# Kernel optimization log

Hardware: AMD Instinct MI355X
Metric: run time of the kernel (lower is better)

Reference implementation:

```python
import jax, jax.numpy as jnp
import numpy as np

MIN_, MAX_, KSZ, IGNORE_IDX = 10, 10, 3, -255
B, H, W = 256, 256, 256
LI_MAX_ITERS = 64


def setup_inputs() -> dict:
    key = jax.random.key(0)
    x = jax.random.uniform(key, (B, 1, H, W), dtype=jnp.float32)
    return {"x": x}


def _otsu(hist):
    # hist: [256] counts. Returns Otsu threshold (bin value); fg = img > t.
    bins = jnp.arange(256, dtype=jnp.float32)
    w0 = jnp.cumsum(hist)[:-1]
    w1 = hist.sum() - w0
    s0 = jnp.cumsum(hist * bins)[:-1]
    s_tot = (hist * bins).sum()
    m0 = s0 / jnp.maximum(w0, 1e-12)
    m1 = (s_tot - s0) / jnp.maximum(w1, 1e-12)
    var_b = w0 * w1 * (m0 - m1) ** 2
    return jnp.argmax(var_b).astype(jnp.float32)


def _li(hist, init_t):
    # Histogram-based Li iterative minimum cross-entropy threshold
    # (skimage.filters.threshold_li with initial_guess=init_t).
    bins = jnp.arange(256, dtype=jnp.float32)
    img_min = jnp.min(jnp.where(hist > 0, bins, 255.0))
    vals = bins - img_min  # shift so values >= 0 (as skimage does)
    csum = jnp.cumsum(hist)
    cvsum = jnp.cumsum(hist * vals)
    n_tot, s_tot = csum[-1], cvsum[-1]
    tol = 0.5  # integer image -> half the minimal value spacing

    def body(state):
        t_curr, _, i = state
        # background: img <= t_curr + img_min
        idx = jnp.clip(jnp.floor(t_curr + img_min).astype(jnp.int32), 0, 255)
        n_back, s_back = csum[idx], cvsum[idx]
        n_fore, s_fore = n_tot - n_back, s_tot - s_back
        mean_back = jnp.where(n_back > 0, s_back / jnp.maximum(n_back, 1.0), 0.0)
        mean_fore = s_fore / jnp.maximum(n_fore, 1.0)
        eps = 1e-12
        t_next = (mean_back - mean_fore) / (
            jnp.log(jnp.maximum(mean_back, eps)) - jnp.log(jnp.maximum(mean_fore, eps)))
        t_next = jnp.where(mean_back < eps, mean_fore / 2.0, t_next)
        return (t_next, t_curr, i + 1)

    def cond(state):
        t_curr, t_prev, i = state
        return (jnp.abs(t_curr - t_prev) > tol) & (i < LI_MAX_ITERS)

    t0 = init_t - img_min
    t_fin, _, _ = jax.lax.while_loop(cond, body, (t0, t0 + 10.0, 0))
    return t_fin + img_min


def _sample_mask(key, region, k):
    # Uniform sampling without replacement of up to k pixels from region
    # (bool [H,W]) via random-score top-k (equiv. to torch.multinomial
    # with uniform probs, w/o replacement).
    flat = region.reshape(-1)
    scores = jnp.where(flat, jax.random.uniform(key, (flat.shape[0],)), -1.0)
    top, idx = jax.lax.top_k(scores, k)
    valid = (top >= 0.0).astype(jnp.int32)
    mask = jnp.zeros(flat.shape[0], jnp.int32).at[idx].max(valid)
    return mask.reshape(region.shape)


def _dilate(m):
    # kornia dilation with ones (KSZ,KSZ) kernel on a 0/1 mask == max filter.
    return jax.lax.reduce_window(m, 0, jax.lax.max, (KSZ, KSZ), (1, 1), "SAME")


def _per_image(img_u8, key_fg, key_bg):
    # img_u8: [H,W] int32 in [0,255]
    hist = jnp.zeros(256, jnp.float32).at[img_u8.ravel()].add(1.0)
    otsu = jnp.clip(_otsu(hist), 1.0, 254.0)  # clamp 0->1, 255->254
    li_t = _li(hist, otsu)
    roi = img_u8.astype(jnp.float32) > li_t

    fg = _sample_mask(key_fg, roi, MAX_)
    bg = _sample_mask(key_bg, jnp.logical_not(roi), MIN_)
    if KSZ > 1:
        fg = _dilate(fg)
        bg = _dilate(bg)

    overlap = (fg + bg) == 2
    fg = jnp.where(overlap, 0, fg)
    bg = jnp.where(overlap, 0, bg)

    seeds = jnp.full((H, W), IGNORE_IDX, jnp.int32)
    seeds = jnp.where(bg == 1, 0, seeds)
    seeds = jnp.where(fg == 1, 1, seeds)
    return seeds


def reference(x):
    b = x.shape[0]
    # (cam*255).astype(uint8): truncation, cam in [0,1]
    img = jnp.clip(jnp.floor(x[:, 0] * 255.0), 0, 255).astype(jnp.int32)
    keys = jax.random.split(jax.random.key(1), (b, 2))
    return jax.vmap(_per_image)(img, keys[:, 0], keys[:, 1])
```

## Files before the change

### kernel.cpp

```cpp
#include <hip/hip_runtime.h>
#include <stdint.h>

#define NPIX 65536
#define IGN (-255)
#define CAPB 96

typedef unsigned long long u64;
typedef int v4i __attribute__((ext_vector_type(4)));

__device__ __forceinline__ uint32_t rotl32(uint32_t v, uint32_t r){ return (v<<r)|(v>>(32u-r)); }

__device__ __forceinline__ void tf2x32(uint32_t k0, uint32_t k1, uint32_t x0, uint32_t x1,
                                       uint32_t &o0, uint32_t &o1){
  uint32_t k2 = k0 ^ k1 ^ 0x1BD11BDAu;
  x0 += k0; x1 += k1;
#define TFR(r) { x0 += x1; x1 = rotl32(x1,(r)); x1 ^= x0; }
  TFR(13u) TFR(15u) TFR(26u) TFR(6u)   x0 += k1; x1 += k2 + 1u;
  TFR(17u) TFR(29u) TFR(16u) TFR(24u)  x0 += k2; x1 += k0 + 2u;
  TFR(13u) TFR(15u) TFR(26u) TFR(6u)   x0 += k0; x1 += k1 + 3u;
  TFR(17u) TFR(29u) TFR(16u) TFR(24u)  x0 += k1; x1 += k2 + 4u;
  TFR(13u) TFR(15u) TFR(26u) TFR(6u)   x0 += k2; x1 += k0 + 5u;
#undef TFR
  o0 = x0; o1 = x1;
}

__device__ __forceinline__ uint32_t tf_bits(uint32_t k0, uint32_t k1, uint32_t k2, uint32_t pix){
  uint32_t x0 = k0, x1 = pix + k1;
#define TFR(r) { x0 += x1; x1 = rotl32(x1,(r)); x1 ^= x0; }
  TFR(13u) TFR(15u) TFR(26u) TFR(6u)   x0 += k1; x1 += k2 + 1u;
  TFR(17u) TFR(29u) TFR(16u) TFR(24u)  x0 += k2; x1 += k0 + 2u;
  TFR(13u) TFR(15u) TFR(26u) TFR(6u)   x0 += k0; x1 += k1 + 3u;
  TFR(17u) TFR(29u) TFR(16u) TFR(24u)  x0 += k1; x1 += k2 + 4u;
  TFR(13u) TFR(15u) TFR(26u) TFR(6u)   x0 += k2; x1 += k0 + 5u;
#undef TFR
  return x0 ^ x1;
}

__device__ __forceinline__ u64 packCand(uint32_t bits, uint32_t pix){
  float f = __uint_as_float((bits >> 9) | 0x3f800000u) - 1.0f;
  uint32_t u = __float_as_uint(f) ^ 0x80000000u;
  return ((u64)u << 32) | (u64)(0xFFFFFFFFu - pix);
}

__device__ __forceinline__ void t10_insert(u64* l, u64 c){
  if (c > l[9]) {
    l[9] = c;
#pragma unroll
    for (int i = 9; i > 0; --i){
      u64 a = l[i-1], b2 = l[i];
      if (b2 > a){ l[i-1] = b2; l[i] = a; }
    }
  }
}

__global__ __launch_bounds__(256)
void k1_hist(const float* __restrict__ x, uint32_t* __restrict__ phist,
             uint32_t* __restrict__ u8c){
  const int img = blockIdx.x >> 3;
  const int chk = blockIdx.x & 7;
  const int tid = threadIdx.x;
  const float4* x4 = (const float4*)(x + (size_t)img * NPIX);

  __shared__ uint32_t h4[1024];
  h4[tid] = 0u; h4[tid+256] = 0u; h4[tid+512] = 0u; h4[tid+768] = 0u;
  __syncthreads();

  const int sub = tid & 3;
#pragma unroll
  for (int j = 0; j < 8; ++j){
    int p4 = chk*2048 + j*256 + tid;
    float4 v = x4[p4];
    uint32_t q0 = (uint32_t)min(max((int)floorf(v.x*255.0f),0),255);
    uint32_t q1 = (uint32_t)min(max((int)floorf(v.y*255.0f),0),255);
    uint32_t q2 = (uint32_t)min(max((int)floorf(v.z*255.0f),0),255);
    uint32_t q3 = (uint32_t)min(max((int)floorf(v.w*255.0f),0),255);
    u8c[(size_t)img*16384 + p4] = q0 | (q1<<8) | (q2<<16) | (q3<<24);
    atomicAdd(&h4[q0*4+sub],1u); atomicAdd(&h4[q1*4+sub],1u);
    atomicAdd(&h4[q2*4+sub],1u); atomicAdd(&h4[q3*4+sub],1u);
  }
  __syncthreads();
  phist[(size_t)(img*8+chk)*256 + tid] = h4[tid*4] + h4[tid*4+1] + h4[tid*4+2] + h4[tid*4+3];
}

__global__ __launch_bounds__(256)
void k1b_thresh(const uint32_t* __restrict__ phist, uint32_t* __restrict__ qcutp,
                uint32_t* __restrict__ nroip){
  const int img = blockIdx.x;
  const int tid = threadIdx.x;

  __shared__ float csum[256], cvsum[256];
  __shared__ u64 s_best;
  __shared__ int s_imin;

  if (tid == 0){ s_imin = 255; s_best = 0ull; }
  uint32_t h = 0;
#pragma unroll
  for (int k = 0; k < 8; ++k) h += phist[(size_t)(img*8+k)*256 + tid];
  __syncthreads();
  if (h) atomicMin(&s_imin, tid);
  __syncthreads();
  const float img_min = (float)s_imin;
  csum[tid]  = (float)h;
  cvsum[tid] = (float)h * ((float)tid - img_min);
  __syncthreads();
  for (int off = 1; off < 256; off <<= 1){
    float a = 0.f, c2 = 0.f;
    if (tid >= off){ a = csum[tid-off]; c2 = cvsum[tid-off]; }
    __syncthreads();
    if (tid >= off){ csum[tid] += a; cvsum[tid] += c2; }
    __syncthreads();
  }
  {
    float s_tot_o = cvsum[255] + img_min * csum[255];
    if (tid < 255){
      float w0 = csum[tid], w1 = 65536.0f - w0;
      float cs = cvsum[tid] + img_min * csum[tid];
      float m0 = cs / fmaxf(w0, 1e-12f);
      float m1 = (s_tot_o - cs) / fmaxf(w1, 1e-12f);
      float d = m0 - m1;
      float vb = (w0*w1) * (d*d);
      u64 pk = ((u64)__float_as_uint(vb) << 32) | (u64)(255 - tid);
      atomicMax(&s_best, pk);
    }
  }
  __syncthreads();
  if (tid == 0){
    int bestIdx = 255 - (int)(s_best & 0xFFFFFFFFull);
    float otsu = fminf(fmaxf((float)bestIdx, 1.0f), 254.0f);
    float n_tot = csum[255], s_tot = cvsum[255];
    float t_curr = otsu - img_min, t_prev = t_curr + 10.0f;
    int it = 0;
    while (fabsf(t_curr - t_prev) > 0.5f && it < 64){
      int idx = min(max((int)floorf(t_curr + img_min), 0), 255);
      float n_back = csum[idx], s_back = cvsum[idx];
      float n_fore = n_tot - n_back, s_fore = s_tot - s_back;
      float mean_back = (n_back > 0.0f) ? (s_back / fmaxf(n_back, 1.0f)) : 0.0f;
      float mean_fore = s_fore / fmaxf(n_fore, 1.0f);
      float t_next = (mean_back - mean_fore) /
                     (logf(fmaxf(mean_back, 1e-12f)) - logf(fmaxf(mean_fore, 1e-12f)));
      if (mean_back < 1e-12f) t_next = mean_fore * 0.5f;
      t_prev = t_curr; t_curr = t_next; ++it;
    }
    float lit = t_curr + img_min;
    int qcut = (int)floorf(lit) + 1;
    uint32_t nroi;
    if (qcut <= 0)        nroi = NPIX;
    else if (qcut > 255)  nroi = 0u;
    else                  nroi = NPIX - (uint32_t)csum[qcut-1];
    qcutp[img] = (uint32_t)qcut;
    nroip[img] = nroi;
  }
}

__global__ __launch_bounds__(256)
void k2_score(const uint32_t* __restrict__ u8c, int* __restrict__ out,
              const uint32_t* __restrict__ qcutp, uint32_t* __restrict__ bcnt,
              u64* __restrict__ cand){
  const int img = blockIdx.x >> 3;
  const int chk = blockIdx.x & 7;
  const int tid = threadIdx.x;

  __shared__ uint32_t s_kw[4], s_cnt[2];
  __shared__ u64 s_cand[2][CAPB];

  if (tid < 2){
    uint32_t o0, o1;
    tf2x32(0u, 1u, 0u, (uint32_t)(2*img + tid), o0, o1);
    s_kw[2*tid] = o0; s_kw[2*tid+1] = o1;
  }
  if (tid == 0){ s_cnt[0] = 0u; s_cnt[1] = 0u; }
  const int qcut = (int)qcutp[img];
  __syncthreads();

  {
    v4i* o4 = (v4i*)(out + (size_t)img * NPIX);
    const v4i f4 = {IGN, IGN, IGN, IGN};
#pragma unroll
    for (int j = 0; j < 8; ++j)
      __builtin_nontemporal_store(f4, &o4[chk*2048 + j*256 + tid]);
  }

  const uint32_t fk0 = s_kw[0], fk1 = s_kw[1], bk0 = s_kw[2], bk1 = s_kw[3];
  const uint32_t fk2 = fk0 ^ fk1 ^ 0x1BD11BDAu;
  const uint32_t bk2 = bk0 ^ bk1 ^ 0x1BD11BDAu;
  const uint4* u4 = (const uint4*)(u8c + (size_t)img*16384);
#pragma unroll
  for (int j = 0; j < 2; ++j){
    int wi = chk*512 + j*256 + tid;
    uint4 w4 = u4[wi];
    uint32_t pix0 = (uint32_t)(wi*16);
    uint32_t ws4[4] = {w4.x, w4.y, w4.z, w4.w};
#pragma unroll
    for (int wsub = 0; wsub < 4; ++wsub){
      uint32_t w = ws4[wsub];
#pragma unroll
      for (int s = 0; s < 4; ++s){
        int q = (int)((w >> (8*s)) & 255u);
        bool r = (q >= qcut);
        uint32_t pix = pix0 + (uint32_t)(wsub*4 + s);
        uint32_t bits = tf_bits(r?fk0:bk0, r?fk1:bk1, r?fk2:bk2, pix);
        if (bits >= 0xFF000000u){
          int r2 = r ? 0 : 1;
          uint32_t idx = atomicAdd(&s_cnt[r2], 1u);
          if (idx < CAPB) s_cand[r2][idx] = packCand(bits, pix);
        }
      }
    }
  }
  __syncthreads();
  if (tid < 2) bcnt[(size_t)(img*8+chk)*2 + tid] = s_cnt[tid];
  {
    int s = tid >> 7, idx = tid & 127;
    int n = min((int)s_cnt[s], CAPB);
    if (idx < n) cand[((size_t)(img*8+chk)*2 + s)*CAPB + idx] = s_cand[s][idx];
  }
}

__global__ __launch_bounds__(256)
void k3_final(const float* __restrict__ x, int* __restrict__ out,
              const uint32_t* __restrict__ qcutp, const uint32_t* __restrict__ nroip,
              const uint32_t* __restrict__ bcnt, const u64* __restrict__ cand){
  const int img = blockIdx.x;
  const int tid = threadIdx.x;

  __shared__ u64 sbuf[2560];
  __shared__ u64 s_top[2][10];
  __shared__ int s_off[2][9], s_fail[2];
  __shared__ uint32_t s_kw[4];
  __shared__ int s_pr[2][10], s_pc[2][10], s_np[2];

  if (tid < 2){
    uint32_t o0, o1;
    tf2x32(0u, 1u, 0u, (uint32_t)(2*img + tid), o0, o1);
    s_kw[2*tid] = o0; s_kw[2*tid+1] = o1;
  }
  if (tid == 0){
    uint32_t nroi = nroip[img];
    for (int s = 0; s < 2; ++s){
      int off = 0, fail = 0;
      for (int k = 0; k < 8; ++k){
        uint32_t raw = bcnt[(size_t)(img*8+k)*2 + s];
        if (raw > (uint32_t)CAPB) fail = 1;
        int ck = (int)min(raw, (uint32_t)CAPB);
        s_off[s][k] = off; off += ck;
      }
      s_off[s][8] = off;
      int region = s ? (int)(NPIX - nroi) : (int)nroi;
      if (off < 10 && off != region) fail = 1;
      s_fail[s] = fail;
    }
  }
  __syncthreads();

  {
    int s = tid >> 7, idx = tid & 127;
#pragma unroll
    for (int k = 0; k < 8; ++k){
      int ck = s_off[s][k+1] - s_off[s][k];
      if (idx < ck) sbuf[s*1280 + s_off[s][k] + idx] = cand[((size_t)(img*8+k)*2 + s)*CAPB + idx];
    }
  }
  __syncthreads();
  if (tid == 0 || tid == 128){
    int s = tid >> 7;
    if (!s_fail[s]){
      u64 t[10];
#pragma unroll
      for (int i = 0; i < 10; ++i) t[i] = 0ull;
      int n = s_off[s][8];
      for (int i = 0; i < n; ++i) t10_insert(t, sbuf[s*1280 + i]);
#pragma unroll
      for (int i = 0; i < 10; ++i) s_top[s][i] = t[i];
    }
  }
  __syncthreads();

  const int qcut = (int)qcutp[img];
  for (int s = 0; s < 2; ++s){
    if (!s_fail[s]) continue;
    uint32_t kk0 = s_kw[2*s], kk1 = s_kw[2*s+1], kk2 = kk0 ^ kk1 ^ 0x1BD11BDAu;
    u64 t[10];
#pragma unroll
    for (int i = 0; i < 10; ++i) t[i] = 0ull;
    for (int k = 0; k < 256; ++k){
      uint32_t pix = (uint32_t)(tid + 256*k);
      float v = x[(size_t)img*NPIX + pix];
      int q = min(max((int)floorf(v*255.0f),0),255);
      bool r = (q >= qcut);
      if (r == (s == 0)) t10_insert(t, packCand(tf_bits(kk0, kk1, kk2, pix), pix));
    }
#pragma unroll
    for (int i = 0; i < 10; ++i) sbuf[tid*10 + i] = t[i];
    __syncthreads();
    if (tid == 0){
      u64 m[10];
#pragma unroll
      for (int i = 0; i < 10; ++i) m[i] = 0ull;
      for (int i = 0; i < 2560; ++i) t10_insert(m, sbuf[i]);
#pragma unroll
      for (int i = 0; i < 10; ++i) s_top[s][i] = m[i];
    }
    __syncthreads();
  }

  if (tid < 2){
    int np = 0;
    for (int i = 0; i < 10; ++i){
      u64 e = s_top[tid][i];
      if (e){
        uint32_t pix = 0xFFFFFFFFu - (uint32_t)(e & 0xFFFFFFFFull);
        s_pr[tid][np] = (int)(pix >> 8);
        s_pc[tid][np] = (int)(pix & 255u);
        ++np;
      }
    }
    s_np[tid] = np;
  }
  __syncthreads();

  int* outb = out + (size_t)img * NPIX;
  const int nfg = s_np[0], nbg = s_np[1];
  const int npts = nfg + nbg;
  if (tid < npts*9){
    int k = tid / 9, d = tid - k*9;
    int pr = (k < nfg) ? s_pr[0][k] : s_pr[1][k - nfg];
    int pc = (k < nfg) ? s_pc[0][k] : s_pc[1][k - nfg];
    pr += d/3 - 1; pc += d%3 - 1;
    if (pr >= 0 && pr < 256 && pc >= 0 && pc < 256){
      bool fgd = false, bgd = false;
      for (int i = 0; i < nfg; ++i) fgd |= (abs(pr - s_pr[0][i]) <= 1) && (abs(pc - s_pc[0][i]) <= 1);
      for (int i = 0; i < nbg; ++i) bgd |= (abs(pr - s_pr[1][i]) <= 1) && (abs(pc - s_pc[1][i]) <= 1);
      int val = (fgd && bgd) ? IGN : (fgd ? 1 : 0);
      outb[pr*256 + pc] = val;
    }
  }
}

__global__ __launch_bounds__(1024, 4)
void apm_fused(const float* __restrict__ x, int* __restrict__ out){
  const int b = blockIdx.x;
  const int tid = threadIdx.x;
  const float* img = x + (size_t)b * NPIX;
  int* outb = out + (size_t)b * NPIX;

  __shared__ uint32_t hist[256];
  __shared__ float csum[256], cvsum[256];
  __shared__ u64 buf[2][256];
  __shared__ uint32_t s_kw[4];
  __shared__ int s_cnt[2];
  __shared__ int s_nroi, s_imin;
  __shared__ u64 s_best;
  __shared__ float s_lit;
  __shared__ int s_fail[2];
  __shared__ int s_pr[2][10], s_pc[2][10], s_np[2];

  if (tid < 256) hist[tid] = 0u;
  if (tid == 0){ s_cnt[0] = 0; s_cnt[1] = 0; s_nroi = 0; s_imin = 255; s_best = 0ull; }
  if (tid < 2){
    uint32_t o0, o1;
    tf2x32(0u, 1u, 0u, (uint32_t)(2*b + tid), o0, o1);
    s_kw[2*tid] = o0; s_kw[2*tid+1] = o1;
  }
  __syncthreads();

  uint32_t packed[16];
  {
    v4i f4 = {IGN, IGN, IGN, IGN};
    const float4* x4 = (const float4*)img;
    v4i* o4 = (v4i*)outb;
#pragma unroll
    for (int j = 0; j < 16; ++j){
      int p4 = tid + 1024*j;
      float4 v = x4[p4];
      o4[p4] = f4;
      uint32_t u0 = (uint32_t)min(max((int)floorf(v.x*255.0f),0),255);
      uint32_t u1 = (uint32_t)min(max((int)floorf(v.y*255.0f),0),255);
      uint32_t u2 = (uint32_t)min(max((int)floorf(v.z*255.0f),0),255);
      uint32_t u3 = (uint32_t)min(max((int)floorf(v.w*255.0f),0),255);
      packed[j] = u0 | (u1<<8) | (u2<<16) | (u3<<24);
      atomicAdd(&hist[u0],1u); atomicAdd(&hist[u1],1u);
      atomicAdd(&hist[u2],1u); atomicAdd(&hist[u3],1u);
    }
  }
  __syncthreads();
  if (tid < 256 && hist[tid]) atomicMin(&s_imin, tid);
  __syncthreads();
  const float img_min = (float)s_imin;
  if (tid < 256){
    float h = (float)hist[tid];
    csum[tid]  = h;
    cvsum[tid] = h * ((float)tid - img_min);
  }
  __syncthreads();
  for (int off = 1; off < 256; off <<= 1){
    float a = 0.f, c2 = 0.f;
    if (tid < 256 && tid >= off){ a = csum[tid-off]; c2 = cvsum[tid-off]; }
    __syncthreads();
    if (tid < 256 && tid >= off){ csum[tid] += a; cvsum[tid] += c2; }
    __syncthreads();
  }
  {
    float s_tot_o = cvsum[255] + img_min * csum[255];
    if (tid < 255){
      float w0 = csum[tid], w1 = 65536.0f - w0;
      float cs = cvsum[tid] + img_min * csum[tid];
      float m0 = cs / fmaxf(w0, 1e-12f);
      float m1 = (s_tot_o - cs) / fmaxf(w1, 1e-12f);
      float d = m0 - m1;
      float vb = (w0*w1) * (d*d);
      u64 pk = ((u64)__float_as_uint(vb) << 32) | (u64)(255 - tid);
      atomicMax(&s_best, pk);
    }
  }
  __syncthreads();
  if (tid == 0){
    int bestIdx = 255 - (int)(s_best & 0xFFFFFFFFull);
    float otsu = fminf(fmaxf((float)bestIdx, 1.0f), 254.0f);
    float n_tot = csum[255], s_tot = cvsum[255];
    float t_curr = otsu - img_min, t_prev = t_curr + 10.0f;
    int it = 0;
    while (fabsf(t_curr - t_prev) > 0.5f && it < 64){
      int idx = min(max((int)floorf(t_curr + img_min), 0), 255);
      float n_back = csum[idx], s_back = cvsum[idx];
      float n_fore = n_tot - n_back, s_fore = s_tot - s_back;
      float mean_back = (n_back > 0.0f) ? (s_back / fmaxf(n_back, 1.0f)) : 0.0f;
      float mean_fore = s_fore / fmaxf(n_fore, 1.0f);
      float t_next = (mean_back - mean_fore) /
                     (logf(fmaxf(mean_back, 1e-12f)) - logf(fmaxf(mean_fore, 1e-12f)));
      if (mean_back < 1e-12f) t_next = mean_fore * 0.5f;
      t_prev = t_curr; t_curr = t_next; ++it;
    }
    s_lit = t_curr + img_min;
  }
  __syncthreads();

  const float lit = s_lit;
  const uint32_t fk0 = s_kw[0], fk1 = s_kw[1], bk0 = s_kw[2], bk1 = s_kw[3];
  const uint32_t THRM = (0xFF000000u >> 9);
  int my_roi = 0;
#pragma unroll
  for (int j = 0; j < 16; ++j){
    uint32_t pk = packed[j];
    uint32_t pix0 = (uint32_t)(4*(tid + 1024*j));
#pragma unroll
    for (int s = 0; s < 4; ++s){
      uint32_t q = (pk >> (8*s)) & 255u;
      bool r = ((float)q > lit);
      my_roi += r ? 1 : 0;
      uint32_t o0, o1;
      tf2x32(r ? fk0 : bk0, r ? fk1 : bk1, 0u, pix0 + (uint32_t)s, o0, o1);
      uint32_t bits = o0 ^ o1;
      if ((bits >> 9) >= THRM){
        int r2 = r ? 0 : 1;
        int idx = atomicAdd(&s_cnt[r2], 1);
        if (idx < 256) buf[r2][idx] = packCand(bits, pix0 + (uint32_t)s);
      }
    }
  }
  for (int off = 32; off; off >>= 1) my_roi += __shfl_down(my_roi, off);
  if ((tid & 63) == 0) atomicAdd(&s_nroi, my_roi);
  __syncthreads();

  if (tid == 0){
    int m0r = s_nroi, m1r = NPIX - s_nroi;
    int c0 = s_cnt[0], c1 = s_cnt[1];
    s_fail[0] = (c0 > 256) || (c0 < 10 && c0 != m0r);
    s_fail[1] = (c1 > 256) || (c1 < 10 && c1 != m1r);
  }
  __syncthreads();

  if (s_fail[0] || s_fail[1]){
    __shared__ u64 smem[640];
    if (tid < 64){
      for (int r2 = 0; r2 < 2; ++r2){
        if (!s_fail[r2]) continue;
        uint32_t kk0 = s_kw[2*r2], kk1 = s_kw[2*r2+1];
        u64 t[10];
#pragma unroll
        for (int i = 0; i < 10; ++i) t[i] = 0ull;
        for (int k2 = 0; k2 < 1024; ++k2){
          uint32_t pix = (uint32_t)(tid + 64*k2);
          float v = img[pix];
          int q = min(max((int)floorf(v*255.0f),0),255);
          bool r = ((float)q > lit);
          if (r != (r2 == 0)) continue;
          uint32_t o0, o1; tf2x32(kk0, kk1, 0u, pix, o0, o1);
          t10_insert(t, packCand(o0 ^ o1, pix));
        }
#pragma unroll
        for (int i = 0; i < 10; ++i) smem[tid*10 + i] = t[i];
      }
    }
    __syncthreads();
    if (tid < 2 && s_fail[tid]){
      u64 t[10];
#pragma unroll
      for (int i = 0; i < 10; ++i) t[i] = 0ull;
      for (int i = 0; i < 640; ++i) t10_insert(t, smem[i]);
#pragma unroll
      for (int i = 0; i < 10; ++i) buf[tid][i] = t[i];
      s_cnt[tid] = 10;
    }
    __syncthreads();
  }

  if (tid == 0 || tid == 64){
    int r2 = (tid == 0) ? 0 : 1;
    int n = min(s_cnt[r2], 256);
    u64 t[10];
#pragma unroll
    for (int i = 0; i < 10; ++i) t[i] = 0ull;
    for (int i = 0; i < n; ++i) t10_insert(t, buf[r2][i]);
    int np = 0;
    for (int i = 0; i < 10; ++i){
      if (t[i]){
        uint32_t pix = 0xFFFFFFFFu - (uint32_t)(t[i] & 0xFFFFFFFFull);
        s_pr[r2][np] = (int)(pix >> 8);
        s_pc[r2][np] = (int)(pix & 255u);
        ++np;
      }
    }
    s_np[r2] = np;
  }
  __syncthreads();

  const int nfg = s_np[0], nbg = s_np[1];
  const int npts = nfg + nbg;
  if (tid < npts*9){
    int k = tid / 9, d = tid - k*9;
    int pr = (k < nfg) ? s_pr[0][k] : s_pr[1][k - nfg];
    int pc = (k < nfg) ? s_pc[0][k] : s_pc[1][k - nfg];
    pr += d/3 - 1; pc += d%3 - 1;
    if (pr >= 0 && pr < 256 && pc >= 0 && pc < 256){
      bool fgd = false, bgd = false;
      for (int i = 0; i < nfg; ++i) fgd |= (abs(pr - s_pr[0][i]) <= 1) && (abs(pc - s_pc[0][i]) <= 1);
      for (int i = 0; i < nbg; ++i) bgd |= (abs(pr - s_pr[1][i]) <= 1) && (abs(pc - s_pc[1][i]) <= 1);
      int val = (fgd && bgd) ? IGN : (fgd ? 1 : 0);
      outb[pr*256 + pc] = val;
    }
  }
}

extern "C" void kernel_launch(void* const* d_in, const int* in_sizes, int n_in,
                              void* d_out, int out_size, void* d_ws, size_t ws_size,
                              hipStream_t stream) {
  const float* x = (const float*)d_in[0];
  int* out = (int*)d_out;
  int B = in_sizes[0] / NPIX;

  size_t cand_b  = (size_t)B * 8 * 2 * CAPB * 8;
  size_t phist_b = (size_t)B * 8 * 256 * 4;
  size_t qcut_b  = (size_t)B * 4;
  size_t nroi_b  = (size_t)B * 4;
  size_t bcnt_b  = (size_t)B * 8 * 2 * 4;
  size_t u8_b    = (size_t)B * 16384 * 4;
  size_t need = cand_b + phist_b + qcut_b + nroi_b + bcnt_b + u8_b;

  if (ws_size < need){
    apm_fused<<<B, 1024, 0, stream>>>(x, out);
    return;
  }
  char* p = (char*)d_ws;
  u64*      cand  = (u64*)p;      p += cand_b;
  uint32_t* phist = (uint32_t*)p; p += phist_b;
  uint32_t* qcutp = (uint32_t*)p; p += qcut_b;
  uint32_t* nroip = (uint32_t*)p; p += nroi_b;
  uint32_t* bcnt  = (uint32_t*)p; p += bcnt_b;
  uint32_t* u8c   = (uint32_t*)p;

  k1_hist   <<<B*8, 256, 0, stream>>>(x, phist, u8c);
  k1b_thresh<<<B,   256, 0, stream>>>(phist, qcutp, nroip);
  k2_score  <<<B*8, 256, 0, stream>>>(u8c, out, qcutp, bcnt, cand);
  k3_final  <<<B,   256, 0, stream>>>(x, out, qcutp, nroip, bcnt, cand);
}
```

Before: 179.9 us.

## Fuse candidate scoring into histogram pass by scoring both keys per pixel

The separate scoring kernel is merged into the histogram kernel. Because the threshold is not yet known at that point, each pixel is hashed with both the foreground and background keys, and its quantized value is packed into the candidate word. The final kernel then filters candidates by region using the stored value. This removes one kernel launch and the write and re-read of the packed u8 image. In exchange it doubles the Threefry work per pixel and raises the chance of candidate overflow, which falls back to the slow full-scan path.

```diff
diff --git a/kernel.cpp b/kernel.cpp
--- a/kernel.cpp
+++ b/kernel.cpp
@@ -42,6 +42,12 @@
   return ((u64)u << 32) | (u64)(0xFFFFFFFFu - pix);
 }
 
+__device__ __forceinline__ u64 packCandQ(uint32_t bits, uint32_t pix, uint32_t q){
+  float f = __uint_as_float((bits >> 9) | 0x3f800000u) - 1.0f;
+  uint32_t u = __float_as_uint(f) ^ 0x80000000u;
+  return ((u64)u << 32) | ((u64)(0xFFFFu - pix) << 16) | (u64)q;
+}
+
 __device__ __forceinline__ void t10_insert(u64* l, u64 c){
   if (c > l[9]) {
     l[9] = c;
@@ -54,32 +60,70 @@
 }
 
 __global__ __launch_bounds__(256)
-void k1_hist(const float* __restrict__ x, uint32_t* __restrict__ phist,
-             uint32_t* __restrict__ u8c){
+void k1_main(const float* __restrict__ x, int* __restrict__ out,
+             uint32_t* __restrict__ phist, uint32_t* __restrict__ bcnt,
+             u64* __restrict__ cand){
   const int img = blockIdx.x >> 3;
   const int chk = blockIdx.x & 7;
   const int tid = threadIdx.x;
   const float4* x4 = (const float4*)(x + (size_t)img * NPIX);
+  v4i* o4 = (v4i*)(out + (size_t)img * NPIX);
 
   __shared__ uint32_t h4[1024];
+  __shared__ uint32_t s_kw[4], s_cnt[2];
+  __shared__ u64 s_cand[2][CAPB];
+
   h4[tid] = 0u; h4[tid+256] = 0u; h4[tid+512] = 0u; h4[tid+768] = 0u;
-  __syncthreads();
-
+  if (tid < 2){
+    uint32_t o0, o1;
+    tf2x32(0u, 1u, 0u, (uint32_t)(2*img + tid), o0, o1);
+    s_kw[2*tid] = o0; s_kw[2*tid+1] = o1;
+  }
+  if (tid == 0){ s_cnt[0] = 0u; s_cnt[1] = 0u; }
+  __syncthreads();
+
+  const uint32_t fk0 = s_kw[0], fk1 = s_kw[1], bk0 = s_kw[2], bk1 = s_kw[3];
+  const uint32_t fk2 = fk0 ^ fk1 ^ 0x1BD11BDAu;
+  const uint32_t bk2 = bk0 ^ bk1 ^ 0x1BD11BDAu;
   const int sub = tid & 3;
+  const v4i f4 = {IGN, IGN, IGN, IGN};
+
 #pragma unroll
   for (int j = 0; j < 8; ++j){
     int p4 = chk*2048 + j*256 + tid;
     float4 v = x4[p4];
+    __builtin_nontemporal_store(f4, &o4[p4]);
     uint32_t q0 = (uint32_t)min(max((int)floorf(v.x*255.0f),0),255);
     uint32_t q1 = (uint32_t)min(max((int)floorf(v.y*255.0f),0),255);
     uint32_t q2 = (uint32_t)min(max((int)floorf(v.z*255.0f),0),255);
     uint32_t q3 = (uint32_t)min(max((int)floorf(v.w*255.0f),0),255);
-    u8c[(size_t)img*16384 + p4] = q0 | (q1<<8) | (q2<<16) | (q3<<24);
     atomicAdd(&h4[q0*4+sub],1u); atomicAdd(&h4[q1*4+sub],1u);
     atomicAdd(&h4[q2*4+sub],1u); atomicAdd(&h4[q3*4+sub],1u);
+    uint32_t pix0 = (uint32_t)(p4*4);
+    uint32_t qq[4] = {q0, q1, q2, q3};
+#pragma unroll
+    for (int s = 0; s < 4; ++s){
+      uint32_t pix = pix0 + (uint32_t)s;
+      uint32_t fb = tf_bits(fk0, fk1, fk2, pix);
+      if (fb >= 0xFF000000u){
+        uint32_t idx = atomicAdd(&s_cnt[0], 1u);
+        if (idx < CAPB) s_cand[0][idx] = packCandQ(fb, pix, qq[s]);
+      }
+      uint32_t bb = tf_bits(bk0, bk1, bk2, pix);
+      if (bb >= 0xFF000000u){
+        uint32_t idx = atomicAdd(&s_cnt[1], 1u);
+        if (idx < CAPB) s_cand[1][idx] = packCandQ(bb, pix, qq[s]);
+      }
+    }
   }
   __syncthreads();
   phist[(size_t)(img*8+chk)*256 + tid] = h4[tid*4] + h4[tid*4+1] + h4[tid*4+2] + h4[tid*4+3];
+  if (tid < 2) bcnt[(size_t)(img*8+chk)*2 + tid] = s_cnt[tid];
+  {
+    int s = tid >> 7, idx = tid & 127;
+    int n = min((int)s_cnt[s], CAPB);
+    if (idx < n) cand[((size_t)(img*8+chk)*2 + s)*CAPB + idx] = s_cand[s][idx];
+  }
 }
 
 __global__ __launch_bounds__(256)
@@ -153,70 +197,6 @@
 }
 
 __global__ __launch_bounds__(256)
-void k2_score(const uint32_t* __restrict__ u8c, int* __restrict__ out,
-              const uint32_t* __restrict__ qcutp, uint32_t* __restrict__ bcnt,
-              u64* __restrict__ cand){
-  const int img = blockIdx.x >> 3;
-  const int chk = blockIdx.x & 7;
-  const int tid = threadIdx.x;
-
-  __shared__ uint32_t s_kw[4], s_cnt[2];
-  __shared__ u64 s_cand[2][CAPB];
-
-  if (tid < 2){
-    uint32_t o0, o1;
-    tf2x32(0u, 1u, 0u, (uint32_t)(2*img + tid), o0, o1);
-    s_kw[2*tid] = o0; s_kw[2*tid+1] = o1;
-  }
-  if (tid == 0){ s_cnt[0] = 0u; s_cnt[1] = 0u; }
-  const int qcut = (int)qcutp[img];
-  __syncthreads();
-
-  {
-    v4i* o4 = (v4i*)(out + (size_t)img * NPIX);
-    const v4i f4 = {IGN, IGN, IGN, IGN};
-#pragma unroll
-    for (int j = 0; j < 8; ++j)
-      __builtin_nontemporal_store(f4, &o4[chk*2048 + j*256 + tid]);
-  }
-
-  const uint32_t fk0 = s_kw[0], fk1 = s_kw[1], bk0 = s_kw[2], bk1 = s_kw[3];
-  const uint32_t fk2 = fk0 ^ fk1 ^ 0x1BD11BDAu;
-  const uint32_t bk2 = bk0 ^ bk1 ^ 0x1BD11BDAu;
-  const uint4* u4 = (const uint4*)(u8c + (size_t)img*16384);
-#pragma unroll
-  for (int j = 0; j < 2; ++j){
-    int wi = chk*512 + j*256 + tid;
-    uint4 w4 = u4[wi];
-    uint32_t pix0 = (uint32_t)(wi*16);
-    uint32_t ws4[4] = {w4.x, w4.y, w4.z, w4.w};
-#pragma unroll
-    for (int wsub = 0; wsub < 4; ++wsub){
-      uint32_t w = ws4[wsub];
-#pragma unroll
-      for (int s = 0; s < 4; ++s){
-        int q = (int)((w >> (8*s)) & 255u);
-        bool r = (q >= qcut);
-        uint32_t pix = pix0 + (uint32_t)(wsub*4 + s);
-        uint32_t bits = tf_bits(r?fk0:bk0, r?fk1:bk1, r?fk2:bk2, pix);
-        if (bits >= 0xFF000000u){
-          int r2 = r ? 0 : 1;
-          uint32_t idx = atomicAdd(&s_cnt[r2], 1u);
-          if (idx < CAPB) s_cand[r2][idx] = packCand(bits, pix);
-        }
-      }
-    }
-  }
-  __syncthreads();
-  if (tid < 2) bcnt[(size_t)(img*8+chk)*2 + tid] = s_cnt[tid];
-  {
-    int s = tid >> 7, idx = tid & 127;
-    int n = min((int)s_cnt[s], CAPB);
-    if (idx < n) cand[((size_t)(img*8+chk)*2 + s)*CAPB + idx] = s_cand[s][idx];
-  }
-}
-
-__global__ __launch_bounds__(256)
 void k3_final(const float* __restrict__ x, int* __restrict__ out,
               const uint32_t* __restrict__ qcutp, const uint32_t* __restrict__ nroip,
               const uint32_t* __restrict__ bcnt, const u64* __restrict__ cand){
@@ -225,7 +205,7 @@
 
   __shared__ u64 sbuf[2560];
   __shared__ u64 s_top[2][10];
-  __shared__ int s_off[2][9], s_fail[2];
+  __shared__ int s_off[2][9], s_ovf[2], s_fail[2], s_nval[2];
   __shared__ uint32_t s_kw[4];
   __shared__ int s_pr[2][10], s_pc[2][10], s_np[2];
 
@@ -234,48 +214,57 @@
     tf2x32(0u, 1u, 0u, (uint32_t)(2*img + tid), o0, o1);
     s_kw[2*tid] = o0; s_kw[2*tid+1] = o1;
   }
+  const int qcut = (int)qcutp[img];
+  if (tid == 0){
+    for (int s = 0; s < 2; ++s){
+      int off = 0, ovf = 0;
+      for (int k = 0; k < 8; ++k){
+        uint32_t raw = bcnt[(size_t)(img*8+k)*2 + s];
+        if (raw > (uint32_t)CAPB) ovf = 1;
+        int ck = (int)min(raw, (uint32_t)CAPB);
+        s_off[s][k] = off; off += ck;
+      }
+      s_off[s][8] = off;
+      s_ovf[s] = ovf;
+    }
+  }
+  __syncthreads();
+
+  {
+    int s = tid >> 7, idx = tid & 127;
+#pragma unroll
+    for (int k = 0; k < 8; ++k){
+      int ck = s_off[s][k+1] - s_off[s][k];
+      if (idx < ck) sbuf[s*1280 + s_off[s][k] + idx] = cand[((size_t)(img*8+k)*2 + s)*CAPB + idx];
+    }
+  }
+  __syncthreads();
+  if (tid == 0 || tid == 128){
+    int s = tid >> 7;
+    u64 t[10];
+#pragma unroll
+    for (int i = 0; i < 10; ++i) t[i] = 0ull;
+    int n = s_off[s][8], nval = 0;
+    for (int i = 0; i < n; ++i){
+      u64 e = sbuf[s*1280 + i];
+      int q = (int)(e & 0xFFull);
+      bool roi = (q >= qcut);
+      if (roi == (s == 0)){ ++nval; t10_insert(t, e); }
+    }
+#pragma unroll
+    for (int i = 0; i < 10; ++i) s_top[s][i] = t[i];
+    s_nval[s] = nval;
+  }
+  __syncthreads();
   if (tid == 0){
     uint32_t nroi = nroip[img];
     for (int s = 0; s < 2; ++s){
-      int off = 0, fail = 0;
-      for (int k = 0; k < 8; ++k){
-        uint32_t raw = bcnt[(size_t)(img*8+k)*2 + s];
-        if (raw > (uint32_t)CAPB) fail = 1;
-        int ck = (int)min(raw, (uint32_t)CAPB);
-        s_off[s][k] = off; off += ck;
-      }
-      s_off[s][8] = off;
       int region = s ? (int)(NPIX - nroi) : (int)nroi;
-      if (off < 10 && off != region) fail = 1;
-      s_fail[s] = fail;
-    }
-  }
-  __syncthreads();
-
-  {
-    int s = tid >> 7, idx = tid & 127;
-#pragma unroll
-    for (int k = 0; k < 8; ++k){
-      int ck = s_off[s][k+1] - s_off[s][k];
-      if (idx < ck) sbuf[s*1280 + s_off[s][k] + idx] = cand[((size_t)(img*8+k)*2 + s)*CAPB + idx];
-    }
-  }
-  __syncthreads();
-  if (tid == 0 || tid == 128){
-    int s = tid >> 7;
-    if (!s_fail[s]){
-      u64 t[10];
-#pragma unroll
-      for (int i = 0; i < 10; ++i) t[i] = 0ull;
-      int n = s_off[s][8];
-      for (int i = 0; i < n; ++i) t10_insert(t, sbuf[s*1280 + i]);
-#pragma unroll
-      for (int i = 0; i < 10; ++i) s_top[s][i] = t[i];
-    }
-  }
-  __syncthreads();
-
-  const int qcut = (int)qcutp[img];
+      s_fail[s] = s_ovf[s] || (s_nval[s] < 10 && s_nval[s] != region);
+    }
+  }
+  __syncthreads();
+
   for (int s = 0; s < 2; ++s){
     if (!s_fail[s]) continue;
     uint32_t kk0 = s_kw[2*s], kk1 = s_kw[2*s+1], kk2 = kk0 ^ kk1 ^ 0x1BD11BDAu;
@@ -287,7 +276,7 @@
       float v = x[(size_t)img*NPIX + pix];
       int q = min(max((int)floorf(v*255.0f),0),255);
       bool r = (q >= qcut);
-      if (r == (s == 0)) t10_insert(t, packCand(tf_bits(kk0, kk1, kk2, pix), pix));
+      if (r == (s == 0)) t10_insert(t, packCandQ(tf_bits(kk0, kk1, kk2, pix), pix, (uint32_t)q));
     }
 #pragma unroll
     for (int i = 0; i < 10; ++i) sbuf[tid*10 + i] = t[i];
@@ -308,7 +297,7 @@
     for (int i = 0; i < 10; ++i){
       u64 e = s_top[tid][i];
       if (e){
-        uint32_t pix = 0xFFFFFFFFu - (uint32_t)(e & 0xFFFFFFFFull);
+        uint32_t pix = 0xFFFFu - (uint32_t)((e >> 16) & 0xFFFFull);
         s_pr[tid][np] = (int)(pix >> 8);
         s_pc[tid][np] = (int)(pix & 255u);
         ++np;
@@ -553,8 +542,7 @@
   size_t qcut_b  = (size_t)B * 4;
   size_t nroi_b  = (size_t)B * 4;
   size_t bcnt_b  = (size_t)B * 8 * 2 * 4;
-  size_t u8_b    = (size_t)B * 16384 * 4;
-  size_t need = cand_b + phist_b + qcut_b + nroi_b + bcnt_b + u8_b;
+  size_t need = cand_b + phist_b + qcut_b + nroi_b + bcnt_b;
 
   if (ws_size < need){
     apm_fused<<<B, 1024, 0, stream>>>(x, out);
@@ -565,11 +553,9 @@
   uint32_t* phist = (uint32_t*)p; p += phist_b;
   uint32_t* qcutp = (uint32_t*)p; p += qcut_b;
   uint32_t* nroip = (uint32_t*)p; p += nroi_b;
-  uint32_t* bcnt  = (uint32_t*)p; p += bcnt_b;
-  uint32_t* u8c   = (uint32_t*)p;
-
-  k1_hist   <<<B*8, 256, 0, stream>>>(x, phist, u8c);
+  uint32_t* bcnt  = (uint32_t*)p;
+
+  k1_main   <<<B*8, 256, 0, stream>>>(x, out, phist, bcnt, cand);
   k1b_thresh<<<B,   256, 0, stream>>>(phist, qcutp, nroip);
-  k2_score  <<<B*8, 256, 0, stream>>>(u8c, out, qcutp, bcnt, cand);
   k3_final  <<<B,   256, 0, stream>>>(x, out, qcutp, nroip, bcnt, cand);
 }
```

Result: slower. 202.4 us (+12.5%).
